# Kernel optimization log

Measured on AMD Instinct MI355X. Metric: run time of the kernel, lower is better.

The kernel has to match this reference:

```python
import jax, jax.numpy as jnp
import numpy as np

N_COUNTRIES = 8
ADJ = jnp.array([
    [0, 1, 1, 1, 1, 1, 1, 0],
    [1, 0, 1, 0, 0, 0, 0, 1],
    [1, 1, 0, 1, 0, 1, 0, 0],
    [1, 0, 1, 0, 1, 1, 1, 0],
    [1, 0, 0, 1, 0, 1, 1, 0],
    [1, 0, 1, 1, 1, 0, 0, 0],
    [1, 0, 0, 1, 1, 0, 0, 0],
    [0, 1, 0, 0, 0, 0, 0, 0]], dtype=jnp.float32)
GDP = jnp.array([0.4, 0.15, 0.12, 0.1, 0.08, 0.08, 0.05, 0.02], dtype=jnp.float32)

B, D_IN, H, NH, L = 8192, 512, 256, 4, 3
HD = H * NH  # 1024: QKV width (no head reshape in the original)


def layer_norm(x, g, b, eps=1e-5):
    m = x.mean(-1, keepdims=True)
    v = ((x - m) ** 2).mean(-1, keepdims=True)
    return (x - m) * jax.lax.rsqrt(v + eps) * g + b


def setup_inputs() -> dict:
    key = jax.random.key(0)
    ks = jax.random.split(key, 12)
    lin = lambda k, i, o: (jax.random.normal(k, (i, o), jnp.float32) / np.sqrt(i).astype(np.float32))
    lin3 = lambda k, i, o: (jax.random.normal(k, (L, i, o), jnp.float32) / np.sqrt(i).astype(np.float32))
    return {
        'regional_features': jax.random.normal(ks[0], (B, D_IN), jnp.float32),
        'Wi': lin(ks[1], D_IN, H), 'bi': jnp.zeros((H,), jnp.float32),
        'emb': 0.02 * jax.random.normal(ks[2], (N_COUNTRIES, H), jnp.float32),
        'Wq': lin3(ks[3], H, HD), 'bq': jnp.zeros((L, HD), jnp.float32),
        'Wk': lin3(ks[4], H, HD), 'bk': jnp.zeros((L, HD), jnp.float32),
        'Wv': lin3(ks[5], H, HD), 'bv': jnp.zeros((L, HD), jnp.float32),
        'Wo': lin3(ks[6], HD, H), 'bo': jnp.zeros((L, H), jnp.float32),
        'ln_g': jnp.ones((L, H), jnp.float32), 'ln_b': jnp.zeros((L, H), jnp.float32),
        'Wp': lin(ks[7], H, H), 'bp': jnp.zeros((H,), jnp.float32),
        'lnp_g': jnp.ones((H,), jnp.float32), 'lnp_b': jnp.zeros((H,), jnp.float32),
    }


def reference(regional_features, Wi, bi, emb, Wq, bq, Wk, bk, Wv, bv, Wo, bo,
              ln_g, ln_b, Wp, bp, lnp_g, lnp_b):
    # input projection + broadcast over the 8 countries + country embedding
    h = regional_features @ Wi + bi                     # [B, H]
    x = h[:, None, :] + emb[None, :, :]                 # [B, 8, H]
    scale = 1.0 / np.sqrt(H).astype(np.float32)         # sqrt(dim)=sqrt(256), as in original
    mask = ADJ == 0                                     # [8, 8]
    for l in range(L):
        Q = x @ Wq[l] + bq[l]                           # [B, 8, HD]
        K = x @ Wk[l] + bk[l]
        V = x @ Wv[l] + bv[l]
        scores = jnp.einsum('bnd,bmd->bnm', Q, K) * scale  # [B, 8, 8]
        scores = jnp.where(mask[None], -jnp.inf, scores)
        attn = jax.nn.softmax(scores, axis=-1)          # dropout is identity in eval
        out = jnp.einsum('bnm,bmd->bnd', attn, V)       # [B, 8, HD]
        out = out @ Wo[l] + bo[l]                       # [B, 8, H]
        x = layer_norm(x + out, ln_g[l], ln_b[l])
    regional = jnp.sum(x * GDP[None, :, None], axis=1)  # [B, H]
    p = layer_norm(regional @ Wp + bp, lnp_g, lnp_b)
    return jax.nn.gelu(p, approximate=False)            # torch nn.GELU default = exact erf
```

## Files before the change

### kernel.cpp

```cpp
#include <hip/hip_runtime.h>
#include <hip/hip_bf16.h>
#include <math.h>


typedef short bf16x8 __attribute__((ext_vector_type(8)));
typedef float f32x4  __attribute__((ext_vector_type(4)));

__device__ __forceinline__ float bflo(unsigned int u){ return __uint_as_float(u << 16); }
__device__ __forceinline__ float bfhi(unsigned int u){ return __uint_as_float(u & 0xffff0000u); }
__device__ __forceinline__ float bfs(short s){ return __uint_as_float((unsigned int)(unsigned short)s << 16); }
__device__ __forceinline__ unsigned short f2bf(float f){
  __hip_bfloat16 h = __float2bfloat16(f);
  return *reinterpret_cast<unsigned short*>(&h);
}
__device__ __forceinline__ int gsw(int r, int q){ return (r + 16*q) ^ (r >> 2); }
__device__ __forceinline__ void unpack8(uint4 a, float* o){
  o[0]=bflo(a.x); o[1]=bfhi(a.x); o[2]=bflo(a.y); o[3]=bfhi(a.y);
  o[4]=bflo(a.z); o[5]=bfhi(a.z); o[6]=bflo(a.w); o[7]=bfhi(a.w);
}
__device__ __forceinline__ uint4 pack8(const float* v){
  uint4 r;
  r.x = (unsigned int)f2bf(v[0]) | ((unsigned int)f2bf(v[1]) << 16);
  r.y = (unsigned int)f2bf(v[2]) | ((unsigned int)f2bf(v[3]) << 16);
  r.z = (unsigned int)f2bf(v[4]) | ((unsigned int)f2bf(v[5]) << 16);
  r.w = (unsigned int)f2bf(v[6]) | ((unsigned int)f2bf(v[7]) << 16);
  return r;
}
__device__ __forceinline__ void gload16(const void* g, void* l){
  __builtin_amdgcn_global_load_lds(
      (const __attribute__((address_space(1))) unsigned int*)g,
      (__attribute__((address_space(3))) unsigned int*)l, 16, 0, 0);
}
__device__ __forceinline__ bf16x8 shfl8(bf16x8 v, int src){
  union U { bf16x8 h; int u[4]; };
  U a, r; a.h = v;
  #pragma unroll
  for (int j = 0; j < 4; j++) r.u[j] = __shfl(a.u[j], src);
  return r.h;
}
__device__ __forceinline__ bf16x8 pk8(const float* v){
  bf16x8 r;
  #pragma unroll
  for (int j = 0; j < 8; j++) r[j] = (short)f2bf(v[j]);
  return r;
}
__device__ __forceinline__ int pidx(int n, int k){
  return (k >> 5)*8192 + (n >> 4)*512 + ((k >> 3) & 3)*128 + (n & 15)*8 + (k & 7);
}

struct P1P {
  const float* csrc[3]; short* cdst[3];
  const float* tsrc[5]; short* tdst[5];
  int trows[5]; int tcols[5]; int tpack[5]; int toff[6];
};
__global__ __launch_bounds__(256) void k_prep1(P1P p){
  __shared__ float tile[64][65];
  int bid = blockIdx.x;
  if (bid < 1152){
    int s = bid / 384, lb = bid % 384;
    size_t e = (size_t)lb * 2048 + (size_t)threadIdx.x * 8;
    const float* src = p.csrc[s] + e;
    float4 v0 = *(const float4*)src;
    float4 v1 = *(const float4*)(src + 4);
    float v[8] = {v0.x,v0.y,v0.z,v0.w,v1.x,v1.y,v1.z,v1.w};
    *(uint4*)(p.cdst[s] + e) = pack8(v);
    return;
  }
  int tb = bid - 1152, s = 0;
  while (tb >= p.toff[s+1]) s++;
  int ti = tb - p.toff[s];
  int cols = p.tcols[s], rows = p.trows[s];
  int ntc = cols >> 6;
  int r0 = (ti / ntc) * 64, c0 = (ti % ntc) * 64;
  const float* src = p.tsrc[s];
  int row = threadIdx.x >> 2, jb = (threadIdx.x & 3) * 16;
  #pragma unroll
  for (int j = 0; j < 16; j += 4){
    float4 v = *(const float4*)(src + (size_t)(r0 + row) * cols + c0 + jb + j);
    tile[row][jb+j] = v.x; tile[row][jb+j+1] = v.y; tile[row][jb+j+2] = v.z; tile[row][jb+j+3] = v.w;
  }
  __syncthreads();
  short* dst = p.tdst[s];
  float tmp[16];
  #pragma unroll
  for (int j = 0; j < 16; j++) tmp[j] = tile[jb + j][row];
  if (p.tpack[s]){
    int n = c0 + row;
    #pragma unroll
    for (int gq = 0; gq < 2; gq++){
      int k = r0 + jb + gq*8;
      *(uint4*)(dst + pidx(n, k)) = pack8(&tmp[gq*8]);
    }
  } else {
    #pragma unroll
    for (int j = 0; j < 16; j += 8)
      *(uint4*)(dst + (size_t)(c0 + row) * rows + r0 + jb + j) = pack8(&tmp[j]);
  }
}

struct GD2 { const short* A; const short* Bt; short* Cp; float scale; };
struct P2P {
  GD2 d[6];
  const short* Wkb; const short* WoTb;
  const float* bq; const float* bv; const float* bo;
  float* ck; float* cvo;
};
__global__ __launch_bounds__(256) void k_prep2(P2P p){
  __shared__ alignas(16) short As[64*128];
  __shared__ alignas(16) short Bs[64*128];
  __shared__ float sv[1024];
  const int bid = blockIdx.x, tid = threadIdx.x;
  if (bid < 96){
    const int lane = tid & 63, w = tid >> 6;
    const int wm = w >> 1, wn = w & 1;
    const int z = bid >> 4, rem = bid & 15, bx = rem >> 2, by = rem & 3;
    GD2 g = p.d[z];
    const int K = 1024;
    f32x4 acc[2][2] = {};
    for (int k0 = 0; k0 < K; k0 += 128){
      #pragma unroll
      for (int kc = 0; kc < 4; kc++){
        int ro = w*16 + (lane & 15);
        int co = k0 + kc*32 + (lane >> 4)*8;
        gload16(g.A  + (size_t)(bx*64 + ro)*K + co, &As[(kc*4 + w)*512]);
        gload16(g.Bt + (size_t)(by*64 + ro)*K + co, &Bs[(kc*4 + w)*512]);
      }
      __syncthreads();
      #pragma unroll
      for (int kc = 0; kc < 4; kc++){
        bf16x8 av[2], bv[2];
        #pragma unroll
        for (int mi = 0; mi < 2; mi++)
          av[mi] = *(const bf16x8*)&As[((kc*4 + wm*2 + mi)*64 + lane)*8];
        #pragma unroll
        for (int nj = 0; nj < 2; nj++)
          bv[nj] = *(const bf16x8*)&Bs[((kc*4 + wn*2 + nj)*64 + lane)*8];
        #pragma unroll
        for (int mi = 0; mi < 2; mi++)
          #pragma unroll
          for (int nj = 0; nj < 2; nj++)
            acc[mi][nj] = __builtin_amdgcn_mfma_f32_16x16x32_bf16(av[mi], bv[nj], acc[mi][nj], 0, 0, 0);
      }
      __syncthreads();
    }
    #pragma unroll
    for (int mi = 0; mi < 2; mi++)
      #pragma unroll
      for (int nj = 0; nj < 2; nj++)
        #pragma unroll
        for (int j = 0; j < 4; j++){
          int r = bx*64 + wm*32 + mi*16 + (lane >> 4)*4 + j;
          int c = by*64 + wn*32 + nj*16 + (lane & 15);
          g.Cp[pidx(r, c)] = (short)f2bf(acc[mi][nj][j] * g.scale);
        }
    return;
  }
  int v = bid - 96;
  int job = v / 3, l = v % 3;
  const short* rows = (job == 0 ? p.Wkb : p.WoTb) + (size_t)l*262144;
  const float* vec  = (job == 0 ? p.bq : p.bv) + l*1024;
  const float scale = (job == 0) ? 0.0625f : 1.0f;
  for (int i = tid; i < 1024; i += 256) sv[i] = vec[i];
  __syncthreads();
  const int row = tid >> 3, sub = tid & 7;
  for (int pass = 0; pass < 8; pass++){
    int r = pass*32 + row;
    const short* rp = rows + (size_t)r*1024;
    float acc = 0.f;
    #pragma unroll
    for (int i = 0; i < 16; i++){
      int d = sub*8 + i*64;
      uint4 vv = *(const uint4*)(rp + d);
      float f[8]; unpack8(vv, f);
      #pragma unroll
      for (int j = 0; j < 8; j++) acc = fmaf(f[j], sv[d + j], acc);
    }
    acc += __shfl_xor(acc, 1); acc += __shfl_xor(acc, 2); acc += __shfl_xor(acc, 4);
    if (sub == 0){
      float o = acc * scale;
      if (job == 1) o += p.bo[l*256 + r];
      (job == 0 ? p.ck : p.cvo)[l*256 + r] = o;
    }
  }
}

__global__ __launch_bounds__(512, 2) void k_net(
    const float* __restrict__ rf, const short* __restrict__ WiT,
    const float* __restrict__ bi, const float* __restrict__ emb,
    const short* __restrict__ Wqk, const short* __restrict__ Wvo,
    const float* __restrict__ ckv, const float* __restrict__ cvov,
    const float* __restrict__ lng, const float* __restrict__ lnb,
    const short* __restrict__ WpT, const float* __restrict__ bpv,
    const float* __restrict__ lpg, const float* __restrict__ lpb,
    float* __restrict__ outp){
  const int tid = threadIdx.x, lane = tid & 63, w = tid >> 6;
  const int b0 = blockIdx.x * 16;
  const int dsub = (lane >> 4) * 8;
  const int glane = gsw(lane & 15, lane >> 4);
  __shared__ alignas(16) short tst[8][2048];
  __shared__ alignas(16) short wbuf[4][4096];
  __shared__ short ckb3[768];
  __shared__ float sadd3[768];
  __shared__ short sg3[768];
  __shared__ short sb3[768];

  #define LKW  asm volatile("s_waitcnt lgkmcnt(0)" ::: "memory")
  #define VMW0 asm volatile("s_waitcnt vmcnt(0)" ::: "memory")
  #define VMW1 asm volatile("s_waitcnt vmcnt(1)" ::: "memory")
  #define VMW2 asm volatile("s_waitcnt vmcnt(2)" ::: "memory")
  #define BAR  __builtin_amdgcn_s_barrier()

  auto STAGE = [&](int n){
    int cc = n & 15;
    const short* W = (((n >> 4) & 1) ? Wvo : Wqk) + (n >> 5)*65536;
    const short* src = W + ((((cc & 7)*16 + (cc >> 3)*8) << 9) + tid*8);
    gload16(src, &wbuf[n & 3][tid*8]);
  };

  float* hst  = (float*)&tst[0][0];
  float* embs = hst + 16*264;
  float* bis  = embs + 2048;
  if (tid < 256) bis[tid] = bi[tid];
  for (int i = tid; i < 2048; i += 512) embs[i] = emb[i];
  f32x4 hacc[2] = {};
  #pragma unroll
  for (int kk = 0; kk < 16; kk++){
    const float* ap = rf + (size_t)(b0 + (lane & 15)) * 512 + kk*32 + dsub;
    float4 a0 = *(const float4*)ap, a1 = *(const float4*)(ap + 4);
    float af[8] = {a0.x,a0.y,a0.z,a0.w,a1.x,a1.y,a1.z,a1.w};
    bf16x8 av = pk8(af);
    #pragma unroll
    for (int nj = 0; nj < 2; nj++){
      bf16x8 bv = *(const bf16x8*)(WiT + (size_t)(kk*16 + w*2 + nj)*512 + lane*8);
      hacc[nj] = __builtin_amdgcn_mfma_f32_16x16x32_bf16(av, bv, hacc[nj], 0, 0, 0);
    }
  }
  for (int i = tid; i < 768; i += 512){
    ckb3[i]  = (short)f2bf(ckv[i]);
    sadd3[i] = cvov[i];
    sg3[i]   = (short)f2bf(lng[i]);
    sb3[i]   = (short)f2bf(lnb[i]);
  }
  __syncthreads();
  #pragma unroll
  for (int nj = 0; nj < 2; nj++)
    #pragma unroll
    for (int jj = 0; jj < 4; jj++){
      int m = (lane >> 4)*4 + jj, col = w*32 + nj*16 + (lane & 15);
      hst[m*264 + col] = hacc[nj][jj] + bis[col];
    }
  __syncthreads();
  bf16x8 xf[8];
  {
    int r15 = lane & 15;
    int bt = w*2 + (r15 >> 3), ct = r15 & 7;
    #pragma unroll
    for (int c = 0; c < 8; c++){
      float v8[8];
      #pragma unroll
      for (int e = 0; e < 8; e++){
        int d = dsub + 32*c + e;
        v8[e] = hst[bt*264 + d] + embs[ct*256 + d];
      }
      xf[c] = pk8(v8);
    }
  }
  VMW0; __syncthreads();
  STAGE(0); STAGE(1); STAGE(2);

  const unsigned long long MASK64 = 0x02191D69752B857EULL;

  #pragma unroll 1
  for (int l = 0; l < 3; ++l){
    const short* ckb  = ckb3  + l*256;
    const float* sadd = sadd3 + l*256;
    const short* sg   = sg3   + l*256;
    const short* sb   = sb3   + l*256;
    const bool lgl = (l == 2);

    f32x4 sacc = {0.f, 0.f, 0.f, 0.f};
    #pragma unroll
    for (int h = 0; h < 2; h++){
      f32x4 acc[8] = {};
      #pragma unroll
      for (int kk = 0; kk < 8; kk++){
        const int n = l*32 + h*8 + kk;
        VMW2; BAR;
        STAGE(n + 3);
        const short* P = &wbuf[n & 3][0];
        #pragma unroll
        for (int nj = 0; nj < 8; nj++){
          bf16x8 bv = *(const bf16x8*)&P[nj*512 + lane*8];
          acc[nj] = __builtin_amdgcn_mfma_f32_16x16x32_bf16(xf[kk], bv, acc[nj], 0, 0, 0);
        }
      }
      #pragma unroll
      for (int nj = 0; nj < 8; nj++)
        #pragma unroll
        for (int jj = 0; jj < 4; jj++){
          int i_ = (lane >> 4)*4 + jj, nl = nj*16 + (lane & 15);
          tst[w][(nl >> 5)*512 + gsw(i_, (nl >> 3) & 3)*8 + (nl & 7)] = (short)f2bf(acc[nj][jj]);
        }
      LKW; __builtin_amdgcn_sched_barrier(0);
      #pragma unroll
      for (int cl = 0; cl < 4; cl++){
        bf16x8 tf = *(const bf16x8*)&tst[w][cl*512 + glane*8];
        sacc = __builtin_amdgcn_mfma_f32_16x16x32_bf16(tf, xf[h*4 + cl], sacc, 0, 0, 0);
      }
      LKW;
    }

    float skv = 0.f;
    #pragma unroll
    for (int c = 0; c < 8; c++){
      bf16x8 cv = *(const bf16x8*)&ckb[c*32 + dsub];
      #pragma unroll
      for (int e = 0; e < 8; e++) skv = fmaf(bfs(xf[c][e]), bfs(cv[e]), skv);
    }
    skv += __shfl_xor(skv, 16); skv += __shfl_xor(skv, 32);

    float* atnw = (float*)&tst[w][0];
    #pragma unroll
    for (int jj = 0; jj < 4; jj++){
      int i_ = (lane >> 4)*4 + jj, j_ = lane & 15;
      bool ok = (((i_ ^ j_) & 8) == 0) &&
                ((MASK64 >> (((i_ & 7) << 3) | (j_ & 7))) & 1ull);
      float sv = ok ? (sacc[jj] + skv) : -3.0e38f;
      float mx = sv;
      mx = fmaxf(mx, __shfl_xor(mx, 1));
      mx = fmaxf(mx, __shfl_xor(mx, 2));
      mx = fmaxf(mx, __shfl_xor(mx, 4));
      float e = ok ? __expf(sv - mx) : 0.f;
      float sum = e;
      sum += __shfl_xor(sum, 1); sum += __shfl_xor(sum, 2); sum += __shfl_xor(sum, 4);
      atnw[i_*16 + j_] = e / sum;
    }
    LKW;

    bf16x8 yfrag[8];
    {
      float4 A0 = *(const float4*)&atnw[(lane & 15)*16 + (lane & 8)];
      float4 A1 = *(const float4*)&atnw[(lane & 15)*16 + (lane & 8) + 4];
      float am[8] = {A0.x, A0.y, A0.z, A0.w, A1.x, A1.y, A1.z, A1.w};
      #pragma unroll
      for (int c = 0; c < 8; c++){
        float a8[8] = {0,0,0,0,0,0,0,0};
        #pragma unroll
        for (int mi = 0; mi < 8; mi++){
          bf16x8 xs = shfl8(xf[c], (lane & 48) | (lane & 8) | mi);
          #pragma unroll
          for (int e = 0; e < 8; e++) a8[e] = fmaf(am[mi], bfs(xs[e]), a8[e]);
        }
        yfrag[c] = pk8(a8);
      }
    }
    LKW;

    float rs = 0.f, rq = 0.f;
    #pragma unroll
    for (int h = 0; h < 2; h++){
      f32x4 acc[8] = {};
      #pragma unroll
      for (int kk = 0; kk < 8; kk++){
        const int c = h*8 + kk;
        const int n = l*32 + 16 + c;
        if (lgl && c == 14){ VMW1; } else if (lgl && c == 15){ VMW0; } else { VMW2; }
        BAR;
        if (!(lgl && c >= 13)) STAGE(n + 3);
        const short* P = &wbuf[n & 3][0];
        #pragma unroll
        for (int nj = 0; nj < 8; nj++){
          bf16x8 bv = *(const bf16x8*)&P[nj*512 + lane*8];
          acc[nj] = __builtin_amdgcn_mfma_f32_16x16x32_bf16(yfrag[kk], bv, acc[nj], 0, 0, 0);
        }
      }
      #pragma unroll
      for (int nj = 0; nj < 8; nj++)
        #pragma unroll
        for (int jj = 0; jj < 4; jj++){
          int i_ = (lane >> 4)*4 + jj;
          int dq = nj*16 + (lane & 15);
          tst[w][(dq >> 5)*512 + gsw(i_, (dq >> 3) & 3)*8 + (dq & 7)] = (short)f2bf(acc[nj][jj]);
        }
      LKW; __builtin_amdgcn_sched_barrier(0);
      #pragma unroll
      for (int lc = 0; lc < 4; lc++){
        int c = h*4 + lc;
        float v8[8];
        #pragma unroll
        for (int e = 0; e < 8; e++){
          int d = 32*c + dsub + e;
          float t = bfs(tst[w][lc*512 + glane*8 + e]) + sadd[d] + bfs(xf[c][e]);
          rs += t; rq = fmaf(t, t, rq);
          v8[e] = t;
        }
        xf[c] = pk8(v8);
      }
      LKW;
    }
    rs += __shfl_xor(rs, 16); rs += __shfl_xor(rs, 32);
    rq += __shfl_xor(rq, 16); rq += __shfl_xor(rq, 32);
    float mn = rs * (1.f/256.f);
    float var = rq * (1.f/256.f) - mn*mn;
    float rr = rsqrtf(fmaxf(var, 0.f) + 1e-5f);
    #pragma unroll
    for (int c = 0; c < 8; c++){
      float v8[8];
      #pragma unroll
      for (int e = 0; e < 8; e++){
        int d = 32*c + dsub + e;
        v8[e] = (bfs(xf[c][e]) - mn) * rr * bfs(sg[d]) + bfs(sb[d]);
      }
      xf[c] = pk8(v8);
    }
  }

  __syncthreads();
  short* Ast = &tst[0][0];
  {
    int c7 = lane & 7;
    float g = (c7 == 0) ? 0.4f : (c7 == 1) ? 0.15f : (c7 == 2) ? 0.12f :
              (c7 == 3) ? 0.1f : (c7 == 4) ? 0.08f : (c7 == 5) ? 0.08f :
              (c7 == 6) ? 0.05f : 0.02f;
    #pragma unroll
    for (int c = 0; c < 8; c++){
      float v8[8];
      #pragma unroll
      for (int e = 0; e < 8; e++){
        float v = g * bfs(xf[c][e]);
        v += __shfl_xor(v, 1); v += __shfl_xor(v, 2); v += __shfl_xor(v, 4);
        v8[e] = v;
      }
      if ((lane & 7) == 0){
        int bt = w*2 + ((lane >> 3) & 1);
        *(bf16x8*)&Ast[bt*264 + dsub + 32*c] = pk8(v8);
      }
    }
  }
  __syncthreads();
  float* redS  = (float*)&tst[6][0];
  float* redQ  = redS + 128;
  float* s_mn  = redQ + 128;
  float* s_rs  = s_mn + 16;
  f32x4 ha[2] = {};
  #pragma unroll
  for (int kk = 0; kk < 8; kk++){
    bf16x8 av = *(const bf16x8*)&Ast[(lane & 15)*264 + kk*32 + dsub];
    #pragma unroll
    for (int nj = 0; nj < 2; nj++){
      bf16x8 bv = *(const bf16x8*)(WpT + (size_t)(kk*16 + w*2 + nj)*512 + lane*8);
      ha[nj] = __builtin_amdgcn_mfma_f32_16x16x32_bf16(av, bv, ha[nj], 0, 0, 0);
    }
  }
  #pragma unroll
  for (int jj = 0; jj < 4; jj++){
    float s = 0.f, q = 0.f;
    #pragma unroll
    for (int nj = 0; nj < 2; nj++){
      int cx = w*32 + nj*16 + (lane & 15);
      float t = ha[nj][jj] + bpv[cx];
      ha[nj][jj] = t;
      s += t; q = fmaf(t, t, q);
    }
    s += __shfl_xor(s, 1); q += __shfl_xor(q, 1);
    s += __shfl_xor(s, 2); q += __shfl_xor(q, 2);
    s += __shfl_xor(s, 4); q += __shfl_xor(q, 4);
    s += __shfl_xor(s, 8); q += __shfl_xor(q, 8);
    if ((lane & 15) == 0){
      int rl = (lane >> 4)*4 + jj;
      redS[w*16 + rl] = s; redQ[w*16 + rl] = q;
    }
  }
  __syncthreads();
  if (tid < 16){
    float sm = 0.f, sq = 0.f;
    #pragma unroll
    for (int w2 = 0; w2 < 8; w2++){ sm += redS[w2*16 + tid]; sq += redQ[w2*16 + tid]; }
    float mn = sm * (1.f/256.f);
    float var = sq * (1.f/256.f) - mn*mn;
    s_mn[tid] = mn;
    s_rs[tid] = rsqrtf(fmaxf(var, 0.f) + 1e-5f);
  }
  __syncthreads();
  #pragma unroll
  for (int jj = 0; jj < 4; jj++){
    int rl = (lane >> 4)*4 + jj;
    float mn = s_mn[rl], rstd = s_rs[rl];
    #pragma unroll
    for (int nj = 0; nj < 2; nj++){
      int cx = w*32 + nj*16 + (lane & 15);
      float y = (ha[nj][jj] - mn) * rstd * lpg[cx] + lpb[cx];
      outp[(size_t)(b0 + rl)*256 + cx] = 0.5f * y * (1.0f + erff(y * 0.70710678118654752f));
    }
  }
  #undef LKW
  #undef VMW0
  #undef VMW1
  #undef VMW2
  #undef BAR
}

extern "C" void kernel_launch(void* const* d_in, const int* in_sizes, int n_in,
                              void* d_out, int out_size, void* d_ws, size_t ws_size,
                              hipStream_t stream){
  (void)in_sizes; (void)n_in; (void)out_size; (void)ws_size;
  const float* rf  = (const float*)d_in[0];
  const float* Wi  = (const float*)d_in[1];
  const float* bi  = (const float*)d_in[2];
  const float* emb = (const float*)d_in[3];
  const float* Wq  = (const float*)d_in[4];
  const float* bq  = (const float*)d_in[5];
  const float* Wk  = (const float*)d_in[6];
  const float* bk  = (const float*)d_in[7];
  const float* Wv  = (const float*)d_in[8];
  const float* bv  = (const float*)d_in[9];
  const float* Wo  = (const float*)d_in[10];
  const float* bo  = (const float*)d_in[11];
  const float* lng = (const float*)d_in[12];
  const float* lnb = (const float*)d_in[13];
  const float* Wp  = (const float*)d_in[14];
  const float* bp  = (const float*)d_in[15];
  const float* lpg = (const float*)d_in[16];
  const float* lpb = (const float*)d_in[17];
  (void)bk;

  char* ws = (char*)d_ws;
  short* Wqb  = (short*)(ws);
  short* Wkb  = (short*)(ws + 1572864ull);
  short* Wvb  = (short*)(ws + 3145728ull);
  short* WoTb = (short*)(ws + 4718592ull);
  short* WqkP = (short*)(ws + 6291456ull);
  short* WvoP = (short*)(ws + 6684672ull);
  short* WiTP = (short*)(ws + 7077888ull);
  short* WpTP = (short*)(ws + 7340032ull);
  float* ckv  = (float*)(ws + 7471104ull);
  float* cvov = (float*)(ws + 7474176ull);

  { P1P p;
    p.csrc[0]=Wq; p.cdst[0]=Wqb;
    p.csrc[1]=Wk; p.cdst[1]=Wkb;
    p.csrc[2]=Wv; p.cdst[2]=Wvb;
    p.tsrc[0]=Wi;        p.tdst[0]=WiTP;          p.trows[0]=512;  p.tcols[0]=256; p.tpack[0]=1;
    p.tsrc[1]=Wo;        p.tdst[1]=WoTb;          p.trows[1]=1024; p.tcols[1]=256; p.tpack[1]=0;
    p.tsrc[2]=Wo+262144; p.tdst[2]=WoTb+262144;   p.trows[2]=1024; p.tcols[2]=256; p.tpack[2]=0;
    p.tsrc[3]=Wo+524288; p.tdst[3]=WoTb+524288;   p.trows[3]=1024; p.tcols[3]=256; p.tpack[3]=0;
    p.tsrc[4]=Wp;        p.tdst[4]=WpTP;          p.trows[4]=256;  p.tcols[4]=256; p.tpack[4]=1;
    p.toff[0]=0; p.toff[1]=32; p.toff[2]=96; p.toff[3]=160; p.toff[4]=224; p.toff[5]=240;
    k_prep1<<<dim3(1392), dim3(256), 0, stream>>>(p); }

  { P2P p;
    for (int l = 0; l < 3; l++){
      p.d[l]   = GD2{ Wkb  + l*262144, Wqb + l*262144, WqkP + l*65536, 0.0625f };
      p.d[3+l] = GD2{ WoTb + l*262144, Wvb + l*262144, WvoP + l*65536, 1.0f };
    }
    p.Wkb = Wkb; p.WoTb = WoTb;
    p.bq = bq; p.bv = bv; p.bo = bo;
    p.ck = ckv; p.cvo = cvov;
    k_prep2<<<dim3(102), dim3(256), 0, stream>>>(p); }

  k_net<<<dim3(512), dim3(512), 0, stream>>>(rf, WiTP, bi, emb, WqkP, WvoP,
      ckv, cvov, lng, lnb, WpTP, bp, lpg, lpb, (float*)d_out);
}
```

Baseline: 212.7 us.

## Halve k_net block to 8 batch rows with 4 waves and triple-buffered weights

Each block of the main fused kernel now handles 8 batch rows with 256 threads instead of 16 rows with 512 threads, so twice as many blocks are launched. Shared memory is cut by using 4 transpose tiles and a 3-deep weight staging ring instead of 4, and the embedding scratch now reuses the weight buffer. The aim is more resident blocks per CU and better load balance. In exchange, each streamed weight chunk is reused across fewer rows, which doubles global weight traffic, and the 16-row MFMA tiles for the input and output projections are now half wasted.

```diff
diff --git a/kernel.cpp b/kernel.cpp
--- a/kernel.cpp
+++ b/kernel.cpp
@@ -184,7 +184,7 @@
   }
 }
 
-__global__ __launch_bounds__(512, 2) void k_net(
+__global__ __launch_bounds__(256, 3) void k_net(
     const float* __restrict__ rf, const short* __restrict__ WiT,
     const float* __restrict__ bi, const float* __restrict__ emb,
     const short* __restrict__ Wqk, const short* __restrict__ Wvo,
@@ -194,11 +194,11 @@
     const float* __restrict__ lpg, const float* __restrict__ lpb,
     float* __restrict__ outp){
   const int tid = threadIdx.x, lane = tid & 63, w = tid >> 6;
-  const int b0 = blockIdx.x * 16;
+  const int b0 = blockIdx.x * 8;
   const int dsub = (lane >> 4) * 8;
   const int glane = gsw(lane & 15, lane >> 4);
-  __shared__ alignas(16) short tst[8][2048];
-  __shared__ alignas(16) short wbuf[4][4096];
+  __shared__ alignas(16) short tst[4][2048];
+  __shared__ alignas(16) short wbuf[3][4096];
   __shared__ short ckb3[768];
   __shared__ float sadd3[768];
   __shared__ short sg3[768];
@@ -206,36 +206,37 @@
 
   #define LKW  asm volatile("s_waitcnt lgkmcnt(0)" ::: "memory")
   #define VMW0 asm volatile("s_waitcnt vmcnt(0)" ::: "memory")
-  #define VMW1 asm volatile("s_waitcnt vmcnt(1)" ::: "memory")
   #define VMW2 asm volatile("s_waitcnt vmcnt(2)" ::: "memory")
   #define BAR  __builtin_amdgcn_s_barrier()
 
   auto STAGE = [&](int n){
     int cc = n & 15;
     const short* W = (((n >> 4) & 1) ? Wvo : Wqk) + (n >> 5)*65536;
-    const short* src = W + ((((cc & 7)*16 + (cc >> 3)*8) << 9) + tid*8);
-    gload16(src, &wbuf[n & 3][tid*8]);
+    const short* src = W + (((cc & 7)*16 + (cc >> 3)*8) << 9);
+    short* dst = &wbuf[n % 3][0];
+    gload16(src + (size_t)tid*8,         dst + tid*8);
+    gload16(src + (size_t)(tid+256)*8,   dst + (tid+256)*8);
   };
 
   float* hst  = (float*)&tst[0][0];
-  float* embs = hst + 16*264;
+  float* embs = (float*)&wbuf[0][0];
   float* bis  = embs + 2048;
-  if (tid < 256) bis[tid] = bi[tid];
-  for (int i = tid; i < 2048; i += 512) embs[i] = emb[i];
-  f32x4 hacc[2] = {};
+  bis[tid] = bi[tid];
+  for (int i = tid; i < 2048; i += 256) embs[i] = emb[i];
+  f32x4 hacc[4] = {};
   #pragma unroll
   for (int kk = 0; kk < 16; kk++){
-    const float* ap = rf + (size_t)(b0 + (lane & 15)) * 512 + kk*32 + dsub;
+    const float* ap = rf + (size_t)(b0 + ((lane & 15) & 7)) * 512 + kk*32 + dsub;
     float4 a0 = *(const float4*)ap, a1 = *(const float4*)(ap + 4);
     float af[8] = {a0.x,a0.y,a0.z,a0.w,a1.x,a1.y,a1.z,a1.w};
     bf16x8 av = pk8(af);
     #pragma unroll
-    for (int nj = 0; nj < 2; nj++){
-      bf16x8 bv = *(const bf16x8*)(WiT + (size_t)(kk*16 + w*2 + nj)*512 + lane*8);
+    for (int nj = 0; nj < 4; nj++){
+      bf16x8 bv = *(const bf16x8*)(WiT + (size_t)(kk*16 + w*4 + nj)*512 + lane*8);
       hacc[nj] = __builtin_amdgcn_mfma_f32_16x16x32_bf16(av, bv, hacc[nj], 0, 0, 0);
     }
   }
-  for (int i = tid; i < 768; i += 512){
+  for (int i = tid; i < 768; i += 256){
     ckb3[i]  = (short)f2bf(ckv[i]);
     sadd3[i] = cvov[i];
     sg3[i]   = (short)f2bf(lng[i]);
@@ -243,11 +244,11 @@
   }
   __syncthreads();
   #pragma unroll
-  for (int nj = 0; nj < 2; nj++)
+  for (int nj = 0; nj < 4; nj++)
     #pragma unroll
     for (int jj = 0; jj < 4; jj++){
-      int m = (lane >> 4)*4 + jj, col = w*32 + nj*16 + (lane & 15);
-      hst[m*264 + col] = hacc[nj][jj] + bis[col];
+      int m = (lane >> 4)*4 + jj, col = w*64 + nj*16 + (lane & 15);
+      if (m < 8) hst[m*264 + col] = hacc[nj][jj] + bis[col];
     }
   __syncthreads();
   bf16x8 xf[8];
@@ -265,8 +266,8 @@
       xf[c] = pk8(v8);
     }
   }
-  VMW0; __syncthreads();
-  STAGE(0); STAGE(1); STAGE(2);
+  LKW; VMW0; __syncthreads();
+  STAGE(0); STAGE(1);
 
   const unsigned long long MASK64 = 0x02191D69752B857EULL;
 
@@ -286,8 +287,8 @@
       for (int kk = 0; kk < 8; kk++){
         const int n = l*32 + h*8 + kk;
         VMW2; BAR;
-        STAGE(n + 3);
-        const short* P = &wbuf[n & 3][0];
+        STAGE(n + 2);
+        const short* P = &wbuf[n % 3][0];
         #pragma unroll
         for (int nj = 0; nj < 8; nj++){
           bf16x8 bv = *(const bf16x8*)&P[nj*512 + lane*8];
@@ -364,10 +365,10 @@
       for (int kk = 0; kk < 8; kk++){
         const int c = h*8 + kk;
         const int n = l*32 + 16 + c;
-        if (lgl && c == 14){ VMW1; } else if (lgl && c == 15){ VMW0; } else { VMW2; }
+        if (lgl && c == 15){ VMW0; } else { VMW2; }
         BAR;
-        if (!(lgl && c >= 13)) STAGE(n + 3);
-        const short* P = &wbuf[n & 3][0];
+        if (!(lgl && c >= 14)) STAGE(n + 2);
+        const short* P = &wbuf[n % 3][0];
         #pragma unroll
         for (int nj = 0; nj < 8; nj++){
           bf16x8 bv = *(const bf16x8*)&P[nj*512 + lane*8];
@@ -438,17 +439,17 @@
     }
   }
   __syncthreads();
-  float* redS  = (float*)&tst[6][0];
-  float* redQ  = redS + 128;
-  float* s_mn  = redQ + 128;
-  float* s_rs  = s_mn + 16;
-  f32x4 ha[2] = {};
+  float* redS = (float*)&tst[2][0];
+  float* redQ = redS + 64;
+  float* s_mn = redQ + 64;
+  float* s_rs = s_mn + 16;
+  f32x4 ha[4] = {};
   #pragma unroll
   for (int kk = 0; kk < 8; kk++){
-    bf16x8 av = *(const bf16x8*)&Ast[(lane & 15)*264 + kk*32 + dsub];
-    #pragma unroll
-    for (int nj = 0; nj < 2; nj++){
-      bf16x8 bv = *(const bf16x8*)(WpT + (size_t)(kk*16 + w*2 + nj)*512 + lane*8);
+    bf16x8 av = *(const bf16x8*)&Ast[((lane & 15) & 7)*264 + kk*32 + dsub];
+    #pragma unroll
+    for (int nj = 0; nj < 4; nj++){
+      bf16x8 bv = *(const bf16x8*)(WpT + (size_t)(kk*16 + w*4 + nj)*512 + lane*8);
       ha[nj] = __builtin_amdgcn_mfma_f32_16x16x32_bf16(av, bv, ha[nj], 0, 0, 0);
     }
   }
@@ -456,8 +457,8 @@
   for (int jj = 0; jj < 4; jj++){
     float s = 0.f, q = 0.f;
     #pragma unroll
-    for (int nj = 0; nj < 2; nj++){
-      int cx = w*32 + nj*16 + (lane & 15);
+    for (int nj = 0; nj < 4; nj++){
+      int cx = w*64 + nj*16 + (lane & 15);
       float t = ha[nj][jj] + bpv[cx];
       ha[nj][jj] = t;
       s += t; q = fmaf(t, t, q);
@@ -468,14 +469,15 @@
     s += __shfl_xor(s, 8); q += __shfl_xor(q, 8);
     if ((lane & 15) == 0){
       int rl = (lane >> 4)*4 + jj;
-      redS[w*16 + rl] = s; redQ[w*16 + rl] = q;
-    }
-  }
-  __syncthreads();
-  if (tid < 16){
+      if (rl < 8){ redS[w*8 + rl] = s; redQ[w*8 + rl] = q; }
+      else       { redS[32 + w*8 + (rl-8)] = s; redQ[32 + w*8 + (rl-8)] = q; }
+    }
+  }
+  __syncthreads();
+  if (tid < 8){
     float sm = 0.f, sq = 0.f;
     #pragma unroll
-    for (int w2 = 0; w2 < 8; w2++){ sm += redS[w2*16 + tid]; sq += redQ[w2*16 + tid]; }
+    for (int w2 = 0; w2 < 4; w2++){ sm += redS[w2*8 + tid]; sq += redQ[w2*8 + tid]; }
     float mn = sm * (1.f/256.f);
     float var = sq * (1.f/256.f) - mn*mn;
     s_mn[tid] = mn;
@@ -485,17 +487,18 @@
   #pragma unroll
   for (int jj = 0; jj < 4; jj++){
     int rl = (lane >> 4)*4 + jj;
-    float mn = s_mn[rl], rstd = s_rs[rl];
-    #pragma unroll
-    for (int nj = 0; nj < 2; nj++){
-      int cx = w*32 + nj*16 + (lane & 15);
-      float y = (ha[nj][jj] - mn) * rstd * lpg[cx] + lpb[cx];
-      outp[(size_t)(b0 + rl)*256 + cx] = 0.5f * y * (1.0f + erff(y * 0.70710678118654752f));
+    if (rl < 8){
+      float mn = s_mn[rl], rstd = s_rs[rl];
+      #pragma unroll
+      for (int nj = 0; nj < 4; nj++){
+        int cx = w*64 + nj*16 + (lane & 15);
+        float y = (ha[nj][jj] - mn) * rstd * lpg[cx] + lpb[cx];
+        outp[(size_t)(b0 + rl)*256 + cx] = 0.5f * y * (1.0f + erff(y * 0.70710678118654752f));
+      }
     }
   }
   #undef LKW
   #undef VMW0
-  #undef VMW1
   #undef VMW2
   #undef BAR
 }
@@ -558,6 +561,6 @@
     p.ck = ckv; p.cvo = cvov;
     k_prep2<<<dim3(102), dim3(256), 0, stream>>>(p); }
 
-  k_net<<<dim3(512), dim3(512), 0, stream>>>(rf, WiTP, bi, emb, WqkP, WvoP,
+  k_net<<<dim3(1024), dim3(256), 0, stream>>>(rf, WiTP, bi, emb, WqkP, WvoP,
       ckv, cvov, lng, lnb, WpTP, bp, lpg, lpb, (float*)d_out);
 }
```

Measured after the change: 251.2 us. 1.18x slower.
